# Optimization experiments

Hardware: AMD Instinct MI355X
Metric: run time of the kernel (lower is better)

Reference implementation:

```python
import jax, jax.numpy as jnp
import numpy as np

PC_RANGE = (-50.0, -50.0, -4.0, 50.0, 50.0, 4.0)
IMG_H, IMG_W = 256.0, 704.0
EPS = 1e-5


def _bilinear_sample(feat, u, v):
    # feat [H,W,C]; u,v [M] in [0,1]; matches F.grid_sample(align_corners=False, padding_mode='zeros')
    H, W, _ = feat.shape
    x = u * W - 0.5
    y = v * H - 0.5
    x0 = jnp.floor(x)
    y0 = jnp.floor(y)
    dx = (x - x0)[:, None]
    dy = (y - y0)[:, None]
    x0 = x0.astype(jnp.int32)
    y0 = y0.astype(jnp.int32)

    def g(xi, yi):
        inb = ((xi >= 0) & (xi < W) & (yi >= 0) & (yi < H)).astype(feat.dtype)[:, None]
        return feat[jnp.clip(yi, 0, H - 1), jnp.clip(xi, 0, W - 1)] * inb

    return (g(x0, y0) * (1 - dx) * (1 - dy) + g(x0 + 1, y0) * dx * (1 - dy)
            + g(x0, y0 + 1) * (1 - dx) * dy + g(x0 + 1, y0 + 1) * dx * dy)


def _conv1x1(t, w, b):
    return jnp.einsum('bchw,oc->bohw', t, w) + b[None, :, None, None]


def _inorm(t, eps=1e-5):
    # InstanceNorm2d (affine=False): normalize per (b, c) over spatial dims
    m = t.mean(axis=(2, 3), keepdims=True)
    var = t.var(axis=(2, 3), keepdims=True)
    return (t - m) * jax.lax.rsqrt(var + eps)


def _forward(feat, lidar2img, bev_pos, pe_w1, pe_b1, pe_w2, pe_b2, pe_w3, pe_b3,
             c1_w, c1_b, c2_w, c2_b, c3_w, c3_b):
    B, N, C, Hf, Wf = feat.shape
    _, P, Hb, Wb, _ = bev_pos.shape
    Q = Hb * Wb
    lo = jnp.asarray(PC_RANGE[:3], feat.dtype)
    hi = jnp.asarray(PC_RANGE[3:], feat.dtype)
    # 'b p h w d -> b (h w) p d', then scale normalized coords into pc_range
    ref01 = jnp.transpose(bev_pos, (0, 2, 3, 1, 4)).reshape(B, Q, P, 3)
    ref = ref01 * (hi - lo) + lo
    # project through per-camera lidar2img (homogeneous)
    pts = jnp.concatenate([ref, jnp.ones_like(ref[..., :1])], axis=-1)  # [B,Q,P,4]
    cam = jnp.einsum('bnij,bqpj->bnqpi', lidar2img, pts)                # [B,N,Q,P,4]
    homo = cam[..., 2]
    z = jnp.maximum(homo, EPS)
    u = cam[..., 0] / z / IMG_W
    v = cam[..., 1] / z / IMG_H
    valid = ((homo > EPS) & (u > 0.0) & (u < 1.0) & (v > 0.0) & (v < 1.0)).astype(feat.dtype)
    # bilinear gather per camera; feats to channel-last ('b n (g c) h w -> (b g) n h w c', G=1)
    fmap = jnp.transpose(feat, (0, 1, 3, 4, 2)).reshape(B * N, Hf, Wf, C)
    samp = jax.vmap(_bilinear_sample)(fmap, u.reshape(B * N, Q * P), v.reshape(B * N, Q * P))
    samp = samp.reshape(B, N, Q, P, C) * valid[..., None]
    samp = samp.sum(axis=1)  # sum over cameras -> [B,Q,P,C]
    # PositionalEncodingMap(3 -> 256 -> 256 -> 128) on normalized reference points
    pe = jax.nn.relu(ref01 @ pe_w1 + pe_b1)
    pe = jax.nn.relu(pe @ pe_w2 + pe_b2)
    pe = pe @ pe_w3 + pe_b3
    samp = samp + pe
    # 'b (h w) g p c -> b (p g c) h w' with g=1
    x = jnp.transpose(samp.reshape(B, Hb, Wb, P, C), (0, 3, 4, 1, 2)).reshape(B, P * C, Hb, Wb)
    gelu = lambda t: jax.nn.gelu(t, approximate=False)
    x = gelu(_inorm(_conv1x1(x, c1_w, c1_b)))
    x = gelu(_inorm(_conv1x1(x, c2_w, c2_b)))
    x = _conv1x1(x, c3_w, c3_b)
    return x


def setup_inputs() -> dict:
    key = jax.random.key(0)
    ks = jax.random.split(key, 16)
    B, N, C, Hf, Wf = 1, 6, 128, 32, 88
    P, Hb, Wb = 4, 160, 160
    E = 128
    MID = 256
    s = 0.02
    return {
        'feat': jax.random.normal(ks[0], (B, N, C, Hf, Wf), jnp.float32),
        'lidar2img': jax.random.normal(ks[1], (B, N, 4, 4), jnp.float32),
        'bev_pos': jax.random.uniform(ks[2], (B, P, Hb, Wb, 3), jnp.float32),
        'pe_w1': jax.random.normal(ks[3], (3, MID), jnp.float32) * s,
        'pe_b1': jnp.zeros((MID,), jnp.float32),
        'pe_w2': jax.random.normal(ks[4], (MID, MID), jnp.float32) * s,
        'pe_b2': jnp.zeros((MID,), jnp.float32),
        'pe_w3': jax.random.normal(ks[5], (MID, E), jnp.float32) * s,
        'pe_b3': jnp.zeros((E,), jnp.float32),
        'c1_w': jax.random.normal(ks[6], (4 * E, P * 128), jnp.float32) * s,
        'c1_b': jnp.zeros((4 * E,), jnp.float32),
        'c2_w': jax.random.normal(ks[7], (E, 4 * E), jnp.float32) * s,
        'c2_b': jnp.zeros((E,), jnp.float32),
        'c3_w': jax.random.normal(ks[8], (E, E), jnp.float32) * s,
        'c3_b': jnp.zeros((E,), jnp.float32),
    }


def reference(feat, lidar2img, bev_pos, pe_w1, pe_b1, pe_w2, pe_b2, pe_w3, pe_b3,
              c1_w, c1_b, c2_w, c2_b, c3_w, c3_b):
    return _forward(feat, lidar2img, bev_pos, pe_w1, pe_b1, pe_w2, pe_b2, pe_w3, pe_b3,
                    c1_w, c1_b, c2_w, c2_b, c3_w, c3_b)
```

## Files before the change

kernel.cpp:

```cpp
#include <hip/hip_runtime.h>
#include <cstdint>
#include <cstddef>

using frag8 = __attribute__((ext_vector_type(8))) short;
using f32x4 = __attribute__((ext_vector_type(4))) float;

__device__ __forceinline__ float b2f_bits(unsigned short u) {
    union { uint32_t u32; float f; } x; x.u32 = ((uint32_t)u) << 16; return x.f;
}
__device__ __forceinline__ float b2f_lo(uint32_t pk) {
    return __builtin_bit_cast(float, pk << 16);
}
__device__ __forceinline__ float b2f_hi(uint32_t pk) {
    return __builtin_bit_cast(float, pk & 0xffff0000u);
}
__device__ __forceinline__ unsigned short f2b(float f) {
    uint32_t u = __builtin_bit_cast(uint32_t, f);
    uint32_t r = (u + 0x7fffu + ((u >> 16) & 1u)) >> 16;
    return (unsigned short)r;
}

#define HF 32
#define WFEAT 88
#define NCAM 6
#define NPT 102400
#define BM 128
#define BN 128
#define BK 64

__global__ __launch_bounds__(256) void k_prep(const float* __restrict__ feat,
                                              const float* __restrict__ pw2,
                                              const float* __restrict__ pw3,
                                              const float* __restrict__ c1w,
                                              const float* __restrict__ c2w,
                                              const float* __restrict__ c3w,
                                              const float* __restrict__ l2i,
                                              const float* __restrict__ bev,
                                              unsigned short* __restrict__ featT,
                                              unsigned short* __restrict__ W2Tb,
                                              unsigned short* __restrict__ W3Tb,
                                              unsigned short* __restrict__ C1Wb,
                                              unsigned short* __restrict__ C2Wb,
                                              unsigned short* __restrict__ C3Wb,
                                              float* __restrict__ stats,
                                              int* __restrict__ poff,
                                              float4* __restrict__ pwts) {
    __shared__ unsigned short tile[64 * 132];
    int b = blockIdx.x, t = threadIdx.x;
    if (b < 2400) {
        int idx = b * 256 + t;
        int n = idx / NPT, pt = idx - n * NPT;
        int q = pt >> 2, p = pt & 3;
        int h = q / 160, w = q - h * 160;
        const float* bv = bev + ((p * 160 + h) * 160 + w) * 3;
        float rx = bv[0] * 100.f - 50.f;
        float ry = bv[1] * 100.f - 50.f;
        float rz = bv[2] * 8.f - 4.f;
        const float* M = l2i + n * 16;
        float c0   = M[0] * rx + M[1] * ry + M[2]  * rz + M[3];
        float c1v  = M[4] * rx + M[5] * ry + M[6]  * rz + M[7];
        float homo = M[8] * rx + M[9] * ry + M[10] * rz + M[11];
        float z = fmaxf(homo, 1e-5f);
        float u = c0 / z / 704.0f;
        float v = c1v / z / 256.0f;
        if (!(homo > 1e-5f && u > 0.f && u < 1.f && v > 0.f && v < 1.f)) {
            poff[idx] = -1;
            return;
        }
        float fx = u * (float)WFEAT - 0.5f;
        float fy = v * (float)HF - 0.5f;
        float fx0 = floorf(fx), fy0 = floorf(fy);
        float dx = fx - fx0, dy = fy - fy0;
        int x0 = (int)fx0, y0 = (int)fy0;
        float wxa = (x0 < 0) ? dx : 1.f - dx;
        float wxb = (x0 >= 0 && x0 < WFEAT - 1) ? dx : 0.f;
        float wya = (y0 < 0) ? dy : 1.f - dy;
        float wyb = (y0 >= 0 && y0 < HF - 1) ? dy : 0.f;
        int bx = max(x0, 0), by = max(y0, 0);
        poff[idx] = ((n * HF + by) * WFEAT + bx) << 7;
        pwts[idx] = make_float4(wxa * wya, wxb * wya, wxa * wyb, wxb * wyb);
        return;
    }
    b -= 2400;
    if (b < 264) {
        int n = b / 44;
        int s0 = (b - n * 44) * 64;
        #pragma unroll
        for (int i = 0; i < 32; ++i) {
            int e = i * 256 + t;
            int c = e >> 6, sl = e & 63;
            tile[sl * 132 + c] = f2b(feat[(size_t)(n * 128 + c) * 2816 + s0 + sl]);
        }
        __syncthreads();
        #pragma unroll
        for (int j = 0; j < 8; ++j) {
            int flat = j * 1024 + t * 4;
            int sl = flat >> 7, c = flat & 127;
            ushort4 v = *(const ushort4*)(tile + sl * 132 + c);
            *(ushort4*)(featT + (size_t)(n * 2816 + s0 + sl) * 128 + c) = v;
        }
        return;
    }
    b -= 264;
    if (b < 256) {
        int idx = b * 256 + t;
        int r = idx >> 8, c = idx & 255;
        W2Tb[c * 256 + r] = f2b(pw2[idx]);
        return;
    }
    b -= 256;
    if (b < 128) {
        int idx = b * 256 + t;
        int r = idx >> 7, c = idx & 127;
        W3Tb[c * 256 + r] = f2b(pw3[idx]);
        return;
    }
    b -= 128;
    if (b < 1024) { int idx = b * 256 + t; C1Wb[idx] = f2b(c1w[idx]); return; }
    b -= 1024;
    if (b < 256)  { int idx = b * 256 + t; C2Wb[idx] = f2b(c2w[idx]); return; }
    b -= 256;
    if (b < 64)   { int idx = b * 256 + t; C3Wb[idx] = f2b(c3w[idx]); return; }
    #pragma unroll
    for (int j = 0; j < 10; ++j) stats[t * 10 + j] = 0.f;
}

__global__ __launch_bounds__(256) void k_sample2(const unsigned short* __restrict__ featT,
                                                 const int* __restrict__ poff,
                                                 const float4* __restrict__ pwts,
                                                 unsigned short* __restrict__ samp) {
    int pt = blockIdx.x * 4 + (threadIdx.x >> 6);
    int lane = threadIdx.x & 63;
    int c2 = lane * 2;
    int offs[NCAM];
    float4 ww[NCAM];
    #pragma unroll
    for (int n = 0; n < NCAM; ++n) offs[n] = poff[n * NPT + pt];
    #pragma unroll
    for (int n = 0; n < NCAM; ++n) ww[n] = pwts[n * NPT + pt];
    float acc0 = 0.f, acc1 = 0.f;
    #pragma unroll
    for (int n = 0; n < NCAM; ++n) {
        if (offs[n] >= 0) {
            const unsigned short* base = featT + offs[n] + c2;
            uint32_t p00 = *(const uint32_t*)(base);
            uint32_t p01 = *(const uint32_t*)(base + 128);
            uint32_t p10 = *(const uint32_t*)(base + WFEAT * 128);
            uint32_t p11 = *(const uint32_t*)(base + WFEAT * 128 + 128);
            float4 w = ww[n];
            acc0 += w.x * b2f_lo(p00) + w.y * b2f_lo(p01) + w.z * b2f_lo(p10) + w.w * b2f_lo(p11);
            acc1 += w.x * b2f_hi(p00) + w.y * b2f_hi(p01) + w.z * b2f_hi(p10) + w.w * b2f_hi(p11);
        }
    }
    uint32_t outpk = (uint32_t)f2b(acc0) | ((uint32_t)f2b(acc1) << 16);
    *(uint32_t*)(samp + (size_t)pt * 128 + c2) = outpk;
}

__device__ __forceinline__ void stage_tile(const unsigned short* __restrict__ g, int ld,
                                           unsigned short* lds, int wave, int lane) {
    #pragma unroll
    for (int j = 0; j < 4; ++j) {
        int idx = wave * 256 + j * 64 + lane;
        int r = idx >> 3;
        int cs = idx & 7;
        int cl = cs ^ (r & 7);
        __builtin_amdgcn_global_load_lds(
            (const __attribute__((address_space(1))) void*)(g + (size_t)r * ld + cl * 8),
            (__attribute__((address_space(3))) void*)(lds + wave * 2048 + j * 512),
            16, 0, 0);
    }
}

__device__ __forceinline__ frag8 frag_read(const unsigned short* lds, int row, int chunk) {
    return *(const frag8*)(lds + row * 64 + ((chunk ^ (row & 7)) << 3));
}

__device__ __forceinline__ void mma_tile(const unsigned short* As, const unsigned short* Bs,
                                         int wm, int wn, int lane, f32x4 (&acc)[4][4]) {
    int lm = lane & 15, lq = lane >> 4;
    #pragma unroll
    for (int kk = 0; kk < 2; ++kk) {
        frag8 a[4], b[4];
        #pragma unroll
        for (int t = 0; t < 4; ++t) a[t] = frag_read(As, wm * 64 + t * 16 + lm, kk * 4 + lq);
        #pragma unroll
        for (int t = 0; t < 4; ++t) b[t] = frag_read(Bs, wn * 64 + t * 16 + lm, kk * 4 + lq);
        #pragma unroll
        for (int tm = 0; tm < 4; ++tm)
            #pragma unroll
            for (int tn = 0; tn < 4; ++tn)
                acc[tm][tn] = __builtin_amdgcn_mfma_f32_16x16x32_bf16(a[tm], b[tn], acc[tm][tn], 0, 0, 0);
    }
}

__global__ __launch_bounds__(256) void k_pe12(const float* __restrict__ bev,
                                              const float* __restrict__ pw1,
                                              const float* __restrict__ pb1,
                                              const unsigned short* __restrict__ Bt,
                                              const float* __restrict__ bias,
                                              unsigned short* __restrict__ H2) {
    __shared__ unsigned short As[BM * BK], Bs[BN * BK];
    __shared__ __align__(16) float wls[4 * 256];
    __shared__ float bevs[3 * 128];
    int t = threadIdx.x, lane = t & 63, wave = t >> 6;
    int wm = wave >> 1, wn = wave & 1;
    int m0 = blockIdx.x * BM, n0 = blockIdx.y * BN;
    {
        int i = t * 4;
        int j = i >> 8, c = i & 255;
        float4 v = (j < 3) ? *(const float4*)(pw1 + j * 256 + c)
                           : *(const float4*)(pb1 + c);
        *(float4*)(wls + i) = v;
    }
    if (t < 128) {
        int m = m0 + t;
        int q = m >> 2, p = m & 3;
        int h = q / 160, w = q - h * 160;
        const float* bv = bev + ((size_t)((p * 160 + h) * 160 + w)) * 3;
        bevs[t] = bv[0]; bevs[128 + t] = bv[1]; bevs[256 + t] = bv[2];
    }
    __syncthreads();
    int r = t & 127;
    int c0 = (t >> 7) * 4;
    float x = bevs[r], y = bevs[128 + r], z = bevs[256 + r];
    f32x4 acc[4][4] = {};
    for (int kt = 0; kt < 4; ++kt) {
        stage_tile(Bt + (size_t)n0 * 256 + kt * BK, 256, Bs, wave, lane);
        #pragma unroll
        for (int j = 0; j < 4; ++j) {
            int cl = c0 + j;
            const float* wp = wls + kt * 64 + cl * 8;
            float4 a0l = *(const float4*)(wp),       a0h = *(const float4*)(wp + 4);
            float4 a1l = *(const float4*)(wp + 256), a1h = *(const float4*)(wp + 260);
            float4 a2l = *(const float4*)(wp + 512), a2h = *(const float4*)(wp + 516);
            float4 bbl = *(const float4*)(wp + 768), bbh = *(const float4*)(wp + 772);
            uint32_t q0 = (uint32_t)f2b(fmaxf(x * a0l.x + y * a1l.x + z * a2l.x + bbl.x, 0.f))
                        | ((uint32_t)f2b(fmaxf(x * a0l.y + y * a1l.y + z * a2l.y + bbl.y, 0.f)) << 16);
            uint32_t q1 = (uint32_t)f2b(fmaxf(x * a0l.z + y * a1l.z + z * a2l.z + bbl.z, 0.f))
                        | ((uint32_t)f2b(fmaxf(x * a0l.w + y * a1l.w + z * a2l.w + bbl.w, 0.f)) << 16);
            uint32_t q2 = (uint32_t)f2b(fmaxf(x * a0h.x + y * a1h.x + z * a2h.x + bbh.x, 0.f))
                        | ((uint32_t)f2b(fmaxf(x * a0h.y + y * a1h.y + z * a2h.y + bbh.y, 0.f)) << 16);
            uint32_t q3 = (uint32_t)f2b(fmaxf(x * a0h.z + y * a1h.z + z * a2h.z + bbh.z, 0.f))
                        | ((uint32_t)f2b(fmaxf(x * a0h.w + y * a1h.w + z * a2h.w + bbh.w, 0.f)) << 16);
            *(uint4*)(As + r * 64 + ((cl ^ (r & 7)) << 3)) = make_uint4(q0, q1, q2, q3);
        }
        __syncthreads();
        mma_tile(As, Bs, wm, wn, lane, acc);
        __syncthreads();
    }
    int lm = lane & 15, lq = lane >> 4;
    #pragma unroll
    for (int tn = 0; tn < 4; ++tn) {
        int n = n0 + wn * 64 + tn * 16 + lm;
        float bn = bias[n];
        #pragma unroll
        for (int tm = 0; tm < 4; ++tm) {
            int mb = m0 + wm * 64 + tm * 16 + lq * 4;
            #pragma unroll
            for (int rr = 0; rr < 4; ++rr)
                H2[(size_t)(mb + rr) * 256 + n] = f2b(fmaxf(acc[tm][tn][rr] + bn, 0.f));
        }
    }
}

__global__ __launch_bounds__(256) void k_gemm_pe3(const unsigned short* __restrict__ A,
                                                  const unsigned short* __restrict__ Bt,
                                                  const float* __restrict__ bias,
                                                  const unsigned short* __restrict__ samp,
                                                  unsigned short* __restrict__ X) {
    __shared__ unsigned short As[BM * BK], Bs[BN * BK];
    int lane = threadIdx.x & 63, wave = threadIdx.x >> 6;
    int wm = wave >> 1, wn = wave & 1;
    int m0 = blockIdx.x * BM;
    f32x4 acc[4][4] = {};
    for (int kt = 0; kt < 4; ++kt) {
        stage_tile(A + (size_t)m0 * 256 + kt * BK, 256, As, wave, lane);
        stage_tile(Bt + (size_t)kt * BK, 256, Bs, wave, lane);
        __syncthreads();
        mma_tile(As, Bs, wm, wn, lane, acc);
        __syncthreads();
    }
    int lm = lane & 15, lq = lane >> 4;
    #pragma unroll
    for (int tn = 0; tn < 4; ++tn) {
        int n = wn * 64 + tn * 16 + lm;
        float bn = bias[n];
        #pragma unroll
        for (int tm = 0; tm < 4; ++tm) {
            int mb = m0 + wm * 64 + tm * 16 + lq * 4;
            #pragma unroll
            for (int rr = 0; rr < 4; ++rr) {
                size_t off = (size_t)(mb + rr) * 128 + n;
                X[off] = f2b(acc[tm][tn][rr] + bn + b2f_bits(samp[off]));
            }
        }
    }
}

template <int K, bool STATS>
__global__ __launch_bounds__(256) void k_gemm_conv(const unsigned short* __restrict__ A,
                                                   const unsigned short* __restrict__ Bt,
                                                   const float* __restrict__ bias,
                                                   unsigned short* __restrict__ Y, int ldY,
                                                   float* __restrict__ st, int C) {
    __shared__ unsigned short As[BM * BK], Bs[BN * BK];
    int lane = threadIdx.x & 63, wave = threadIdx.x >> 6;
    int wm = wave >> 1, wn = wave & 1;
    int m0 = blockIdx.x * BM, n0 = blockIdx.y * BN;
    f32x4 acc[4][4] = {};
    for (int kt = 0; kt < K / BK; ++kt) {
        stage_tile(A + (size_t)m0 * K + kt * BK, K, As, wave, lane);
        stage_tile(Bt + (size_t)n0 * K + kt * BK, K, Bs, wave, lane);
        __syncthreads();
        mma_tile(As, Bs, wm, wn, lane, acc);
        __syncthreads();
    }
    int lm = lane & 15, lq = lane >> 4;
    #pragma unroll
    for (int tn = 0; tn < 4; ++tn) {
        int n = n0 + wn * 64 + tn * 16 + lm;
        float bn = bias[n];
        float s1 = 0.f, s2 = 0.f;
        #pragma unroll
        for (int tm = 0; tm < 4; ++tm) {
            int mb = m0 + wm * 64 + tm * 16 + lq * 4;
            #pragma unroll
            for (int rr = 0; rr < 4; ++rr) {
                float v = acc[tm][tn][rr] + bn;
                Y[(size_t)(mb + rr) * ldY + n] = f2b(v);
                if (STATS) { s1 += v; s2 += v * v; }
            }
        }
        if (STATS) {
            s1 += __shfl_xor(s1, 16); s1 += __shfl_xor(s1, 32);
            s2 += __shfl_xor(s2, 16); s2 += __shfl_xor(s2, 32);
            if (lq == 0) { atomicAdd(&st[n], s1); atomicAdd(&st[C + n], s2); }
        }
    }
}

__global__ __launch_bounds__(256) void k_gemm_conv3(const unsigned short* __restrict__ A,
                                                    const unsigned short* __restrict__ Bt,
                                                    const float* __restrict__ bias,
                                                    float* __restrict__ out) {
    __shared__ unsigned short As[BM * BK], Bs[BN * BK];
    int lane = threadIdx.x & 63, wave = threadIdx.x >> 6;
    int wm = wave >> 1, wn = wave & 1;
    int m0 = blockIdx.x * BM;
    f32x4 acc[4][4] = {};
    for (int kt = 0; kt < 2; ++kt) {
        stage_tile(A + (size_t)m0 * 128 + kt * BK, 128, As, wave, lane);
        stage_tile(Bt + (size_t)kt * BK, 128, Bs, wave, lane);
        __syncthreads();
        mma_tile(As, Bs, wm, wn, lane, acc);
        __syncthreads();
    }
    int lm = lane & 15, lq = lane >> 4;
    #pragma unroll
    for (int tn = 0; tn < 4; ++tn) {
        int n = wn * 64 + tn * 16 + lm;
        float bn = bias[n];
        #pragma unroll
        for (int tm = 0; tm < 4; ++tm) {
            int mb = m0 + wm * 64 + tm * 16 + lq * 4;
            float4 pk;
            pk.x = acc[tm][tn][0] + bn;
            pk.y = acc[tm][tn][1] + bn;
            pk.z = acc[tm][tn][2] + bn;
            pk.w = acc[tm][tn][3] + bn;
            *(float4*)(out + (size_t)n * 25600 + mb) = pk;
        }
    }
}

__global__ void k_normgelu8f(const unsigned short* __restrict__ Y, const float* __restrict__ st,
                             unsigned short* __restrict__ X2, int Cmask, int C, float inv_n,
                             int total8) {
    int i8 = blockIdx.x * 256 + threadIdx.x;
    if (i8 >= total8) return;
    int e0 = i8 * 8;
    int c = e0 & Cmask;
    uint4 y = *(const uint4*)(Y + e0);
    float4 s1a = *(const float4*)(st + c);
    float4 s1b = *(const float4*)(st + c + 4);
    float4 s2a = *(const float4*)(st + C + c);
    float4 s2b = *(const float4*)(st + C + c + 4);
    float mu[8] = { s1a.x * inv_n, s1a.y * inv_n, s1a.z * inv_n, s1a.w * inv_n,
                    s1b.x * inv_n, s1b.y * inv_n, s1b.z * inv_n, s1b.w * inv_n };
    float sq[8] = { s2a.x, s2a.y, s2a.z, s2a.w, s2b.x, s2b.y, s2b.z, s2b.w };
    float rs[8];
    #pragma unroll
    for (int j = 0; j < 8; ++j) rs[j] = rsqrtf(sq[j] * inv_n - mu[j] * mu[j] + 1e-5f);
    const float is2 = 0.70710678118654752f;
    unsigned int yw[4] = {y.x, y.y, y.z, y.w};
    unsigned int ow[4];
    #pragma unroll
    for (int j = 0; j < 4; ++j) {
        float v0 = (b2f_bits((unsigned short)(yw[j] & 0xffffu)) - mu[j * 2]) * rs[j * 2];
        float v1 = (b2f_bits((unsigned short)(yw[j] >> 16)) - mu[j * 2 + 1]) * rs[j * 2 + 1];
        float g0 = 0.5f * v0 * (1.f + erff(v0 * is2));
        float g1 = 0.5f * v1 * (1.f + erff(v1 * is2));
        ow[j] = (uint32_t)f2b(g0) | ((uint32_t)f2b(g1) << 16);
    }
    *(uint4*)(X2 + e0) = make_uint4(ow[0], ow[1], ow[2], ow[3]);
}

extern "C" void kernel_launch(void* const* d_in, const int* in_sizes, int n_in,
                              void* d_out, int out_size, void* d_ws, size_t ws_size,
                              hipStream_t stream) {
    (void)in_sizes; (void)n_in; (void)out_size; (void)ws_size;
    const float* feat = (const float*)d_in[0];
    const float* l2i  = (const float*)d_in[1];
    const float* bev  = (const float*)d_in[2];
    const float* pw1  = (const float*)d_in[3];
    const float* pb1  = (const float*)d_in[4];
    const float* pw2  = (const float*)d_in[5];
    const float* pb2  = (const float*)d_in[6];
    const float* pw3  = (const float*)d_in[7];
    const float* pb3  = (const float*)d_in[8];
    const float* c1w  = (const float*)d_in[9];
    const float* c1b  = (const float*)d_in[10];
    const float* c2w  = (const float*)d_in[11];
    const float* c2b  = (const float*)d_in[12];
    const float* c3w  = (const float*)d_in[13];
    const float* c3b  = (const float*)d_in[14];
    float* outp = (float*)d_out;
    char* ws = (char*)d_ws;

    unsigned short* featT = (unsigned short*)(ws + 0);
    unsigned short* W2Tb  = (unsigned short*)(ws + 4348416);
    unsigned short* W3Tb  = (unsigned short*)(ws + 4479488);
    unsigned short* C1Wb  = (unsigned short*)(ws + 4545024);
    unsigned short* C2Wb  = (unsigned short*)(ws + 5069312);
    unsigned short* C3Wb  = (unsigned short*)(ws + 5200384);
    float* stats          = (float*)(ws + 5233152);
    int*    poff          = (int*)(ws + 5247488);
    float4* pwts          = (float4*)(ws + 7705088);
    char* BUF1 = ws + 17535488;
    char* BUF2 = ws + 69964288;
    char* BUF3 = ws + 122393088;

    float* st512 = stats;
    float* st128 = stats + 2048;

    unsigned short* H2   = (unsigned short*)BUF2;
    unsigned short* samp = (unsigned short*)BUF3;
    unsigned short* X    = (unsigned short*)BUF1;
    unsigned short* Y1   = (unsigned short*)BUF2;
    unsigned short* X2   = (unsigned short*)BUF3;
    unsigned short* Y2   = (unsigned short*)BUF1;
    unsigned short* X3   = (unsigned short*)(BUF1 + 6553600);

    k_prep<<<4393, 256, 0, stream>>>(feat, pw2, pw3, c1w, c2w, c3w, l2i, bev,
                                     featT, W2Tb, W3Tb, C1Wb, C2Wb, C3Wb, stats,
                                     poff, pwts);

    k_sample2<<<25600, 256, 0, stream>>>(featT, poff, pwts, samp);

    k_pe12<<<dim3(800, 2), 256, 0, stream>>>(bev, pw1, pb1, W2Tb, pb2, H2);
    k_gemm_pe3<<<dim3(800, 1), 256, 0, stream>>>(H2, W3Tb, pb3, samp, X);

    k_gemm_conv<512, true><<<dim3(200, 4), 256, 0, stream>>>(X, C1Wb, c1b, Y1, 512, st512, 512);
    k_normgelu8f<<<6400, 256, 0, stream>>>(Y1, st512, X2, 511, 512, 1.f / 25600.f, 1638400);

    k_gemm_conv<512, true><<<dim3(200, 1), 256, 0, stream>>>(X2, C2Wb, c2b, Y2, 128, st128, 128);
    k_normgelu8f<<<1600, 256, 0, stream>>>(Y2, st128, X3, 127, 128, 1.f / 25600.f, 409600);

    k_gemm_conv3<<<dim3(200, 1), 256, 0, stream>>>(X3, C3Wb, c3b, outp);
}
```

Before: 278.5 us.

## Double-buffer LDS tiles in GEMM kernels and use hardware bf16 pack conversion

Replaces the single-buffered stage/sync/mma loop in the pe3, conv and conv3 GEMMs with a two-stage LDS double buffer. The next K tile's global loads are issued while the current tile is multiplied, synchronised with explicit vmcnt/lgkmcnt waits and raw barriers. Separately, the first PE layer's bf16 packing switches from software rounding to the v_cvt_pk_bf16_f32 instruction. LDS use per block doubles, which can lower occupancy, and the hand-written vmcnt(8) relies on stage_tile issuing a specific number of loads.

```diff
diff --git a/kernel.cpp b/kernel.cpp
--- a/kernel.cpp
+++ b/kernel.cpp
@@ -18,6 +18,11 @@
     uint32_t u = __builtin_bit_cast(uint32_t, f);
     uint32_t r = (u + 0x7fffu + ((u >> 16) & 1u)) >> 16;
     return (unsigned short)r;
+}
+__device__ __forceinline__ uint32_t cvtpk_bf16(float lo, float hi) {
+    uint32_t r;
+    asm("v_cvt_pk_bf16_f32 %0, %1, %2" : "=v"(r) : "v"(lo), "v"(hi));
+    return r;
 }
 
 #define HF 32
@@ -193,6 +198,59 @@
     }
 }
 
+template <int KT>
+__device__ __forceinline__ void gemm_loop_pipe(const unsigned short* __restrict__ A, int ldA,
+                                               const unsigned short* __restrict__ B, int ldB,
+                                               unsigned short (*As)[BM * BK],
+                                               unsigned short (*Bs)[BN * BK],
+                                               int wave, int lane, int wm, int wn,
+                                               f32x4 (&acc)[4][4]) {
+    stage_tile(A, ldA, As[0], wave, lane);
+    stage_tile(B, ldB, Bs[0], wave, lane);
+    if (KT > 1) {
+        stage_tile(A + BK, ldA, As[1], wave, lane);
+        stage_tile(B + BK, ldB, Bs[1], wave, lane);
+    }
+    #pragma unroll
+    for (int kt = 0; kt < KT; ++kt) {
+        int cur = kt & 1;
+        if (kt + 1 < KT) asm volatile("s_waitcnt vmcnt(8)" ::: "memory");
+        else             asm volatile("s_waitcnt vmcnt(0)" ::: "memory");
+        __builtin_amdgcn_s_barrier();
+        mma_tile(As[cur], Bs[cur], wm, wn, lane, acc);
+        asm volatile("s_waitcnt lgkmcnt(0)" ::: "memory");
+        __builtin_amdgcn_s_barrier();
+        if (kt + 2 < KT) {
+            stage_tile(A + (kt + 2) * BK, ldA, As[cur], wave, lane);
+            stage_tile(B + (kt + 2) * BK, ldB, Bs[cur], wave, lane);
+        }
+    }
+}
+
+__device__ __forceinline__ void build_h1(const float* __restrict__ wls, float x, float y, float z,
+                                         int r, int c0, int kt, unsigned short* __restrict__ As) {
+    #pragma unroll
+    for (int j = 0; j < 4; ++j) {
+        int cl = c0 + j;
+        const float* wp = wls + kt * 64 + cl * 8;
+        float4 a0l = *(const float4*)(wp),       a0h = *(const float4*)(wp + 4);
+        float4 a1l = *(const float4*)(wp + 256), a1h = *(const float4*)(wp + 260);
+        float4 a2l = *(const float4*)(wp + 512), a2h = *(const float4*)(wp + 516);
+        float4 bbl = *(const float4*)(wp + 768), bbh = *(const float4*)(wp + 772);
+        float v0 = fmaxf(x * a0l.x + y * a1l.x + z * a2l.x + bbl.x, 0.f);
+        float v1 = fmaxf(x * a0l.y + y * a1l.y + z * a2l.y + bbl.y, 0.f);
+        float v2 = fmaxf(x * a0l.z + y * a1l.z + z * a2l.z + bbl.z, 0.f);
+        float v3 = fmaxf(x * a0l.w + y * a1l.w + z * a2l.w + bbl.w, 0.f);
+        float v4 = fmaxf(x * a0h.x + y * a1h.x + z * a2h.x + bbh.x, 0.f);
+        float v5 = fmaxf(x * a0h.y + y * a1h.y + z * a2h.y + bbh.y, 0.f);
+        float v6 = fmaxf(x * a0h.z + y * a1h.z + z * a2h.z + bbh.z, 0.f);
+        float v7 = fmaxf(x * a0h.w + y * a1h.w + z * a2h.w + bbh.w, 0.f);
+        uint32_t q0 = cvtpk_bf16(v0, v1), q1 = cvtpk_bf16(v2, v3);
+        uint32_t q2 = cvtpk_bf16(v4, v5), q3 = cvtpk_bf16(v6, v7);
+        *(uint4*)(As + r * 64 + ((cl ^ (r & 7)) << 3)) = make_uint4(q0, q1, q2, q3);
+    }
+}
+
 __global__ __launch_bounds__(256) void k_pe12(const float* __restrict__ bev,
                                               const float* __restrict__ pw1,
                                               const float* __restrict__ pb1,
@@ -226,24 +284,7 @@
     f32x4 acc[4][4] = {};
     for (int kt = 0; kt < 4; ++kt) {
         stage_tile(Bt + (size_t)n0 * 256 + kt * BK, 256, Bs, wave, lane);
-        #pragma unroll
-        for (int j = 0; j < 4; ++j) {
-            int cl = c0 + j;
-            const float* wp = wls + kt * 64 + cl * 8;
-            float4 a0l = *(const float4*)(wp),       a0h = *(const float4*)(wp + 4);
-            float4 a1l = *(const float4*)(wp + 256), a1h = *(const float4*)(wp + 260);
-            float4 a2l = *(const float4*)(wp + 512), a2h = *(const float4*)(wp + 516);
-            float4 bbl = *(const float4*)(wp + 768), bbh = *(const float4*)(wp + 772);
-            uint32_t q0 = (uint32_t)f2b(fmaxf(x * a0l.x + y * a1l.x + z * a2l.x + bbl.x, 0.f))
-                        | ((uint32_t)f2b(fmaxf(x * a0l.y + y * a1l.y + z * a2l.y + bbl.y, 0.f)) << 16);
-            uint32_t q1 = (uint32_t)f2b(fmaxf(x * a0l.z + y * a1l.z + z * a2l.z + bbl.z, 0.f))
-                        | ((uint32_t)f2b(fmaxf(x * a0l.w + y * a1l.w + z * a2l.w + bbl.w, 0.f)) << 16);
-            uint32_t q2 = (uint32_t)f2b(fmaxf(x * a0h.x + y * a1h.x + z * a2h.x + bbh.x, 0.f))
-                        | ((uint32_t)f2b(fmaxf(x * a0h.y + y * a1h.y + z * a2h.y + bbh.y, 0.f)) << 16);
-            uint32_t q3 = (uint32_t)f2b(fmaxf(x * a0h.z + y * a1h.z + z * a2h.z + bbh.z, 0.f))
-                        | ((uint32_t)f2b(fmaxf(x * a0h.w + y * a1h.w + z * a2h.w + bbh.w, 0.f)) << 16);
-            *(uint4*)(As + r * 64 + ((cl ^ (r & 7)) << 3)) = make_uint4(q0, q1, q2, q3);
-        }
+        build_h1(wls, x, y, z, r, c0, kt, As);
         __syncthreads();
         mma_tile(As, Bs, wm, wn, lane, acc);
         __syncthreads();
@@ -268,18 +309,12 @@
                                                   const float* __restrict__ bias,
                                                   const unsigned short* __restrict__ samp,
                                                   unsigned short* __restrict__ X) {
-    __shared__ unsigned short As[BM * BK], Bs[BN * BK];
+    __shared__ unsigned short As[2][BM * BK], Bs[2][BN * BK];
     int lane = threadIdx.x & 63, wave = threadIdx.x >> 6;
     int wm = wave >> 1, wn = wave & 1;
     int m0 = blockIdx.x * BM;
     f32x4 acc[4][4] = {};
-    for (int kt = 0; kt < 4; ++kt) {
-        stage_tile(A + (size_t)m0 * 256 + kt * BK, 256, As, wave, lane);
-        stage_tile(Bt + (size_t)kt * BK, 256, Bs, wave, lane);
-        __syncthreads();
-        mma_tile(As, Bs, wm, wn, lane, acc);
-        __syncthreads();
-    }
+    gemm_loop_pipe<4>(A + (size_t)m0 * 256, 256, Bt, 256, As, Bs, wave, lane, wm, wn, acc);
     int lm = lane & 15, lq = lane >> 4;
     #pragma unroll
     for (int tn = 0; tn < 4; ++tn) {
@@ -303,18 +338,13 @@
                                                    const float* __restrict__ bias,
                                                    unsigned short* __restrict__ Y, int ldY,
                                                    float* __restrict__ st, int C) {
-    __shared__ unsigned short As[BM * BK], Bs[BN * BK];
+    __shared__ unsigned short As[2][BM * BK], Bs[2][BN * BK];
     int lane = threadIdx.x & 63, wave = threadIdx.x >> 6;
     int wm = wave >> 1, wn = wave & 1;
     int m0 = blockIdx.x * BM, n0 = blockIdx.y * BN;
     f32x4 acc[4][4] = {};
-    for (int kt = 0; kt < K / BK; ++kt) {
-        stage_tile(A + (size_t)m0 * K + kt * BK, K, As, wave, lane);
-        stage_tile(Bt + (size_t)n0 * K + kt * BK, K, Bs, wave, lane);
-        __syncthreads();
-        mma_tile(As, Bs, wm, wn, lane, acc);
-        __syncthreads();
-    }
+    gemm_loop_pipe<K / BK>(A + (size_t)m0 * K, K, Bt + (size_t)n0 * K, K,
+                           As, Bs, wave, lane, wm, wn, acc);
     int lm = lane & 15, lq = lane >> 4;
     #pragma unroll
     for (int tn = 0; tn < 4; ++tn) {
@@ -343,18 +373,12 @@
                                                     const unsigned short* __restrict__ Bt,
                                                     const float* __restrict__ bias,
                                                     float* __restrict__ out) {
-    __shared__ unsigned short As[BM * BK], Bs[BN * BK];
+    __shared__ unsigned short As[2][BM * BK], Bs[2][BN * BK];
     int lane = threadIdx.x & 63, wave = threadIdx.x >> 6;
     int wm = wave >> 1, wn = wave & 1;
     int m0 = blockIdx.x * BM;
     f32x4 acc[4][4] = {};
-    for (int kt = 0; kt < 2; ++kt) {
-        stage_tile(A + (size_t)m0 * 128 + kt * BK, 128, As, wave, lane);
-        stage_tile(Bt + (size_t)kt * BK, 128, Bs, wave, lane);
-        __syncthreads();
-        mma_tile(As, Bs, wm, wn, lane, acc);
-        __syncthreads();
-    }
+    gemm_loop_pipe<2>(A + (size_t)m0 * 128, 128, Bt, 128, As, Bs, wave, lane, wm, wn, acc);
     int lm = lane & 15, lq = lane >> 4;
     #pragma unroll
     for (int tn = 0; tn < 4; ++tn) {
@@ -466,5 +490,5 @@
     k_gemm_conv<512, true><<<dim3(200, 1), 256, 0, stream>>>(X2, C2Wb, c2b, Y2, 128, st128, 128);
     k_normgelu8f<<<1600, 256, 0, stream>>>(Y2, st128, X3, 127, 128, 1.f / 25600.f, 409600);
 
-    k_gemm_conv3<<<dim3(200, 1), 256, 0, stream>>>(X3, C3Wb, c3b, outp);
-}
+    k_gemm_conv3<<<200, 256, 0, stream>>>(X3, C3Wb, c3b, outp);
+}
```

New measurement: 269.9 us. 1.03x faster.
